# Kernel optimization log

Measured on AMD Instinct MI355X. Metric: run time of the kernel, lower is better.

The kernel has to match this reference:

```python
import math
import jax, jax.numpy as jnp
import numpy as np

NUM_HEADS = 16
NEG = -1e30  # block-causal 'invisible' value (stand-in for -inf)
SCALES = [(1, 1, 1), (1, 2, 2), (1, 4, 4), (1, 8, 8), (1, 16, 16), (1, 32, 32)]


def _block_causal_bias(L):
    blocks = np.array([t * h * w for (t, h, w) in SCALES])
    cum = np.cumsum(blocks)  # visible kv length for each scale block
    per_query_visible = np.repeat(cum, blocks)  # (L,)
    cols = np.arange(L)
    mask = np.where(cols[None, :] < per_query_visible[:, None], 0.0, NEG).astype(np.float32)
    return jnp.asarray(mask)[None, None]  # (1,1,L,L)


def _rope_tables(L, half_dim):
    # 2D-rope-style cos/sin tables; exact frequency layout is data, math is the rotation
    pos = np.arange(L, dtype=np.float32)
    inv_freq = 1.0 / (10000.0 ** (np.arange(half_dim, dtype=np.float32) / half_dim))
    ang = pos[:, None] * inv_freq[None, :]  # (L, half_dim)
    return jnp.asarray(np.cos(ang)), jnp.asarray(np.sin(ang))


def setup_inputs() -> dict:
    key = jax.random.key(0)
    ks = jax.random.split(key, 6)
    B, C, H = 4, 1024, NUM_HEADS
    hd = C // H
    L = int(sum(t * h * w for (t, h, w) in SCALES))  # 1365
    x = jax.random.normal(ks[0], (B, L, C), dtype=jnp.float32)
    attn_bias = _block_causal_bias(L)
    rope_cos, rope_sin = _rope_tables(L, hd // 2)
    W_qkv = jax.random.normal(ks[1], (3 * C, C), dtype=jnp.float32) * (C ** -0.5)
    q_bias = jnp.zeros((C,), dtype=jnp.float32)
    v_bias = jnp.zeros((C,), dtype=jnp.float32)
    scale_mul_log = jnp.full((1, H, 1, 1), math.log(4.0), dtype=jnp.float32)
    W_proj = jax.random.normal(ks[2], (C, C), dtype=jnp.float32) * (C ** -0.5)
    b_proj = jnp.zeros((C,), dtype=jnp.float32)
    return {"x": x, "attn_bias": attn_bias, "rope_cos": rope_cos, "rope_sin": rope_sin,
            "W_qkv": W_qkv, "q_bias": q_bias, "v_bias": v_bias,
            "scale_mul_log": scale_mul_log, "W_proj": W_proj, "b_proj": b_proj}


def _apply_rope(t, rope_cos, rope_sin):
    # t: (B,H,L,hd) -> rotate consecutive pairs with per-position cos/sin
    B, H, L, hd = t.shape
    t2 = t.reshape(B, H, L, hd // 2, 2)
    c = rope_cos[None, None]  # (1,1,L,hd/2)
    s = rope_sin[None, None]
    r0 = c * t2[..., 0] - s * t2[..., 1]
    r1 = s * t2[..., 0] + c * t2[..., 1]
    return jnp.stack([r0, r1], axis=-1).reshape(B, H, L, hd)


def reference(x, attn_bias, rope_cos, rope_sin, W_qkv, q_bias, v_bias,
              scale_mul_log, W_proj, b_proj):
    B, L, C = x.shape
    H = NUM_HEADS
    hd = C // H
    # QKV with custom bias construction: (q_bias, zeros, v_bias)
    bias = jnp.concatenate([q_bias, jnp.zeros_like(q_bias), v_bias])
    qkv = (x @ W_qkv.T + bias).reshape(B, L, 3, H, hd)
    qkv = jnp.transpose(qkv, (2, 0, 3, 1, 4))  # (3,B,H,L,hd)
    q, k, v = qkv[0], qkv[1], qkv[2]
    # cos-attn: L2-normalize q,k; q scaled by clamped learnable per-head temperature
    max_scale_mul = math.log(100.0)
    scale_mul = jnp.exp(jnp.minimum(scale_mul_log, max_scale_mul))  # (1,H,1,1)
    q = q / jnp.maximum(jnp.linalg.norm(q, axis=-1, keepdims=True), 1e-12) * scale_mul
    k = k / jnp.maximum(jnp.linalg.norm(k, axis=-1, keepdims=True), 1e-12)
    # inline RoPE on q and k
    q = _apply_rope(q, rope_cos, rope_sin)
    k = _apply_rope(k, rope_cos, rope_sin)
    # block-causal attention; softmax scale = 1 under cos_attn
    logits = jnp.einsum('bhqd,bhkd->bhqk', q, k) + attn_bias
    attn = jax.nn.softmax(logits, axis=-1)
    out = jnp.einsum('bhqk,bhkd->bhqd', attn, v)
    out = jnp.transpose(out, (0, 2, 1, 3)).reshape(B, L, C)
    return out @ W_proj.T + b_proj
```

## Files before the change

### kernel.cpp

```cpp
#include <hip/hip_runtime.h>

typedef __bf16 bf16_t;
typedef __bf16 bf16x8 __attribute__((ext_vector_type(8)));
typedef float f32x4 __attribute__((ext_vector_type(4)));

#define B_SZ 4
#define NHEADS 16
#define L_SEQ 1365
#define LP_V 1408
#define C_DIM 1024
#define HD 64
#define M_ROWS (B_SZ * L_SEQ)
#define K_DIM 1024
#define BHL (B_SZ * NHEADS * L_SEQ)

#define NSPLIT 33
#define NCHUNK 2
#define UPB (10 + NSPLIT * NCHUNK)
#define NBLK_ATTN (64 * UPB / 4)

__device__ __forceinline__ f32x4 zero4() {
    f32x4 z; z[0] = 0.f; z[1] = 0.f; z[2] = 0.f; z[3] = 0.f; return z;
}

__device__ __forceinline__ void gload_lds16(const void* g, void* l) {
    __builtin_amdgcn_global_load_lds(
        (const __attribute__((address_space(1))) void*)(uintptr_t)g,
        (__attribute__((address_space(3))) void*)(unsigned int)(uintptr_t)l,
        16, 0, 0);
}

__device__ __forceinline__ int vislen(int row) {
    if (row < 1) return 1;
    if (row < 5) return 5;
    if (row < 21) return 21;
    if (row < 85) return 85;
    if (row < 341) return 341;
    return 1365;
}

#define N8_X  (5591040 / 8)
#define N8_WQ (3145728 / 8)
#define N8_WP (1048576 / 8)
__global__ __launch_bounds__(256) void cvt_all(const float* __restrict__ x,
                                               const float* __restrict__ wq,
                                               const float* __restrict__ wp,
                                               bf16_t* __restrict__ xo,
                                               bf16_t* __restrict__ wqo,
                                               bf16_t* __restrict__ wpo) {
    int i = blockIdx.x * 256 + threadIdx.x;
    const float* in;
    bf16_t* out;
    if (i < N8_X) { in = x; out = xo; }
    else if (i < N8_X + N8_WQ) { i -= N8_X; in = wq; out = wqo; }
    else if (i < N8_X + N8_WQ + N8_WP) { i -= N8_X + N8_WQ; in = wp; out = wpo; }
    else return;
    const float* p = in + (size_t)i * 8;
    f32x4 a = *(const f32x4*)p;
    f32x4 b = *(const f32x4*)(p + 4);
    bf16x8 r;
    r[0] = (bf16_t)a[0]; r[1] = (bf16_t)a[1]; r[2] = (bf16_t)a[2]; r[3] = (bf16_t)a[3];
    r[4] = (bf16_t)b[0]; r[5] = (bf16_t)b[1]; r[6] = (bf16_t)b[2]; r[7] = (bf16_t)b[3];
    *(bf16x8*)(out + (size_t)i * 8) = r;
}

__global__ __launch_bounds__(256) void qkv_gemm(const bf16_t* __restrict__ A,
                                                const bf16_t* __restrict__ Bw,
                                                const float* __restrict__ qbias,
                                                const float* __restrict__ vbias,
                                                const float* __restrict__ rc,
                                                const float* __restrict__ rs,
                                                const float* __restrict__ sml,
                                                bf16_t* __restrict__ qo,
                                                bf16_t* __restrict__ ko,
                                                bf16_t* __restrict__ vt) {
    __shared__ __align__(16) bf16_t As[128 * 32];
    __shared__ __align__(16) bf16_t Bs[128 * 32];
    const int tid = threadIdx.x;
    const int w = tid >> 6, lane = tid & 63, quad = lane >> 4, l16 = lane & 15;
    const int id = blockIdx.x;
    const int xcd = id & 7, s = id >> 3;
    const int ntile = xcd * 3 + s / 43;
    const int mtile = s - (s / 43) * 43;
    const int mw = (w >> 1) * 64, nw = (w & 1) * 64;

    int ar0 = mtile * 128 + (tid >> 2); if (ar0 > M_ROWS - 1) ar0 = M_ROWS - 1;
    int ar1 = ar0 + 64;                 if (ar1 > M_ROWS - 1) ar1 = M_ROWS - 1;
    const int nr0 = ntile * 128 + (tid >> 2);
    const int cc = (tid & 3) * 8;

    f32x4 acc[4][4];
#pragma unroll
    for (int i = 0; i < 4; ++i)
#pragma unroll
        for (int j = 0; j < 4; ++j) acc[i][j] = zero4();

    for (int k0 = 0; k0 < K_DIM; k0 += 32) {
        __syncthreads();
        gload_lds16(A + (size_t)ar0 * K_DIM + k0 + cc, (char*)As + tid * 16);
        gload_lds16(A + (size_t)ar1 * K_DIM + k0 + cc, (char*)As + tid * 16 + 4096);
        gload_lds16(Bw + (size_t)nr0 * K_DIM + k0 + cc, (char*)Bs + tid * 16);
        gload_lds16(Bw + (size_t)(nr0 + 64) * K_DIM + k0 + cc, (char*)Bs + tid * 16 + 4096);
        __syncthreads();
        bf16x8 af[4], bfr[4];
#pragma unroll
        for (int mi = 0; mi < 4; ++mi)
            af[mi] = *(const bf16x8*)&As[(mw + mi * 16 + l16) * 32 + quad * 8];
#pragma unroll
        for (int ni = 0; ni < 4; ++ni)
            bfr[ni] = *(const bf16x8*)&Bs[(nw + ni * 16 + l16) * 32 + quad * 8];
#pragma unroll
        for (int mi = 0; mi < 4; ++mi)
#pragma unroll
            for (int ni = 0; ni < 4; ++ni)
                acc[mi][ni] = __builtin_amdgcn_mfma_f32_16x16x32_bf16(af[mi], bfr[ni], acc[mi][ni], 0, 0, 0);
    }

    const int three = ntile >> 3;
    const int h = (((ntile & 7) * 128 + nw) >> 6);

    if (three == 2) {
#pragma unroll
        for (int ni = 0; ni < 4; ++ni) {
            int d = ni * 16 + l16;
            float bv = vbias[h * 64 + d];
#pragma unroll
            for (int mi = 0; mi < 4; ++mi)
#pragma unroll
                for (int r = 0; r < 4; ++r) {
                    int grow = mtile * 128 + mw + mi * 16 + quad * 4 + r;
                    if (grow < M_ROWS) {
                        int b_ = grow / L_SEQ;
                        int l = grow - b_ * L_SEQ;
                        vt[(((size_t)(b_ * NHEADS + h)) * L_SEQ + l) * HD + d] =
                            (bf16_t)(acc[mi][ni][r] + bv);
                    }
                }
        }
    } else {
        float scale = 1.f;
        if (three == 0) scale = __expf(fminf(sml[h], 4.6051702f));
        float bias[4];
#pragma unroll
        for (int ni = 0; ni < 4; ++ni)
            bias[ni] = (three == 0) ? qbias[h * 64 + ni * 16 + l16] : 0.f;
        bf16_t* dst = (three == 0) ? qo : ko;
#pragma unroll
        for (int mi = 0; mi < 4; ++mi)
#pragma unroll
            for (int r = 0; r < 4; ++r) {
                int grow = mtile * 128 + mw + mi * 16 + quad * 4 + r;
                float vv[4];
                float ss = 0.f;
#pragma unroll
                for (int ni = 0; ni < 4; ++ni) {
                    vv[ni] = acc[mi][ni][r] + bias[ni];
                    ss += vv[ni] * vv[ni];
                }
                ss += __shfl_xor(ss, 1); ss += __shfl_xor(ss, 2);
                ss += __shfl_xor(ss, 4); ss += __shfl_xor(ss, 8);
                float inv = scale * rsqrtf(fmaxf(ss, 1e-24f));
                int gc = grow < M_ROWS ? grow : M_ROWS - 1;
                int b_ = gc / L_SEQ;
                int l = gc - b_ * L_SEQ;
#pragma unroll
                for (int ni = 0; ni < 4; ++ni) {
                    float vn = vv[ni] * inv;
                    float pp = __shfl_xor(vn, 1);
                    int ti = l * 32 + ni * 8 + (l16 >> 1);
                    float c = rc[ti], s2 = rs[ti];
                    float ov = (l16 & 1) ? (s2 * pp + c * vn) : (c * vn - s2 * pp);
                    if (grow < M_ROWS)
                        dst[(((size_t)(b_ * NHEADS + h)) * L_SEQ + l) * HD + ni * 16 + l16] =
                            (bf16_t)ov;
                }
            }
    }
}

__global__ __launch_bounds__(256) void vtrans(const bf16_t* __restrict__ in,
                                              bf16_t* __restrict__ out) {
    __shared__ bf16_t t[64][64];
    const int lt = blockIdx.x * 64, bh = blockIdx.y;
    const int tid = threadIdx.x;
#pragma unroll
    for (int it = 0; it < 2; ++it) {
        const int r = (tid >> 3) + it * 32, c8 = (tid & 7) * 8;
        int l = lt + r; if (l > L_SEQ - 1) l = L_SEQ - 1;
        bf16x8 v8 = *(const bf16x8*)(in + ((size_t)bh * L_SEQ + l) * HD + c8);
#pragma unroll
        for (int j = 0; j < 8; ++j) t[c8 + j][r] = v8[j];
    }
    __syncthreads();
#pragma unroll
    for (int it = 0; it < 2; ++it) {
        int c = tid + it * 256;
        int d = c >> 3, off = (c & 7) * 8;
        bf16x8 o8 = *(const bf16x8*)&t[d][off];
        *(bf16x8*)(out + ((size_t)bh * HD + d) * LP_V + lt + off) = o8;
    }
}

__global__ __launch_bounds__(256) void attn(const bf16_t* __restrict__ q,
                                            const bf16_t* __restrict__ k,
                                            const bf16_t* __restrict__ v,
                                            bf16_t* __restrict__ ao,
                                            float* __restrict__ OP,
                                            float* __restrict__ LPb) {
    __shared__ __align__(16) bf16_t plds[4][2][16][72];
    const int tid = threadIdx.x;
    const int w = tid >> 6, lane = tid & 63, quad = lane >> 4, l16 = lane & 15;
    const int bid = blockIdx.x;
    const int xcd = bid & 7, s0 = bid >> 3;
    const int bh = (xcd << 3) + s0 / 19;
    const int ublk = s0 - (s0 / 19) * 19;
    const int u = ublk * 4 + w;
    int g, t0, t1, ck = 0;
    bool direct;
    if (u < 10) { g = u; t0 = 0; t1 = (u < 2) ? 2 : 6; direct = true; }
    else {
        int t = u - 10;
        int gi = t >> 1;
        ck = t & 1;
        g = 10 + gi;
        t0 = ck * 11;
        t1 = t0 + 11;
        direct = false;
    }
    const int qbase = g * 32;

    bf16x8 aq[2][2];
#pragma unroll
    for (int h = 0; h < 2; ++h) {
        int mrow = qbase + h * 16 + l16;
        int mc = mrow < L_SEQ ? mrow : (L_SEQ - 1);
        const bf16_t* qp = q + ((size_t)bh * L_SEQ + mc) * HD + quad * 8;
        aq[h][0] = *(const bf16x8*)(qp);
        aq[h][1] = *(const bf16x8*)(qp + 32);
    }

    f32x4 o[2][4];
    float l_i[2][4];
    int visr[2][4];
#pragma unroll
    for (int h = 0; h < 2; ++h)
#pragma unroll
        for (int r = 0; r < 4; ++r) {
            o[h][r] = zero4();
            l_i[h][r] = 0.f;
            visr[h][r] = vislen(qbase + h * 16 + quad * 4 + r);
        }

    for (int kt = t0; kt < t1; ++kt) {
        const int kvb = kt * 64;
        bf16x8 kf0[4], kf1[4];
#pragma unroll
        for (int nb = 0; nb < 4; ++nb) {
            int n = kvb + nb * 16 + l16;
            int nc = n < L_SEQ ? n : (L_SEQ - 1);
            const bf16_t* kp = k + ((size_t)bh * L_SEQ + nc) * HD + quad * 8;
            kf0[nb] = *(const bf16x8*)(kp);
            kf1[nb] = *(const bf16x8*)(kp + 32);
        }
        f32x4 s[2][4];
#pragma unroll
        for (int h = 0; h < 2; ++h)
#pragma unroll
            for (int nb = 0; nb < 4; ++nb) {
                s[h][nb] = zero4();
                s[h][nb] = __builtin_amdgcn_mfma_f32_16x16x32_bf16(aq[h][0], kf0[nb], s[h][nb], 0, 0, 0);
                s[h][nb] = __builtin_amdgcn_mfma_f32_16x16x32_bf16(aq[h][1], kf1[nb], s[h][nb], 0, 0, 0);
            }

#pragma unroll
        for (int h = 0; h < 2; ++h)
#pragma unroll
            for (int nb = 0; nb < 4; ++nb) {
                int col = kvb + nb * 16 + l16;
#pragma unroll
                for (int r = 0; r < 4; ++r) {
                    float e = __expf(s[h][nb][r]);
                    float p = (col < visr[h][r]) ? e : 0.f;
                    l_i[h][r] += p;
                    plds[w][h][quad * 4 + r][nb * 16 + l16] = (bf16_t)p;
                }
            }
        bf16x8 ap[2][2];
#pragma unroll
        for (int h = 0; h < 2; ++h) {
            ap[h][0] = *(const bf16x8*)&plds[w][h][l16][quad * 8];
            ap[h][1] = *(const bf16x8*)&plds[w][h][l16][32 + quad * 8];
        }
#pragma unroll
        for (int nb = 0; nb < 4; ++nb) {
            const bf16_t* vp = v + ((size_t)bh * HD + nb * 16 + l16) * LP_V + kvb + quad * 8;
            bf16x8 v0 = *(const bf16x8*)(vp);
            bf16x8 v1 = *(const bf16x8*)(vp + 32);
#pragma unroll
            for (int h = 0; h < 2; ++h) {
                o[h][nb] = __builtin_amdgcn_mfma_f32_16x16x32_bf16(ap[h][0], v0, o[h][nb], 0, 0, 0);
                o[h][nb] = __builtin_amdgcn_mfma_f32_16x16x32_bf16(ap[h][1], v1, o[h][nb], 0, 0, 0);
            }
        }
    }

    if (direct) {
        const int b_ = bh >> 4, hh = bh & 15;
#pragma unroll
        for (int h = 0; h < 2; ++h)
#pragma unroll
            for (int r = 0; r < 4; ++r) {
                float ls = l_i[h][r];
#pragma unroll
                for (int off = 1; off < 16; off <<= 1) ls += __shfl_xor(ls, off);
                int rowq = qbase + h * 16 + quad * 4 + r;
                if (rowq < L_SEQ) {
                    float inv = 1.f / ls;
#pragma unroll
                    for (int nb = 0; nb < 4; ++nb) {
                        int d = nb * 16 + l16;
                        size_t di = ((size_t)(b_ * L_SEQ + rowq)) * C_DIM + hh * HD + d;
                        ao[di] = (bf16_t)(o[h][nb][r] * inv);
                    }
                }
            }
    } else {
        const int g9 = g - 10;
        size_t ub = (((size_t)ck * 64 + bh) * NSPLIT + g9) * 2048;
#pragma unroll
        for (int h = 0; h < 2; ++h)
#pragma unroll
            for (int nb = 0; nb < 4; ++nb)
                *(f32x4*)(OP + ub + (size_t)((h * 4 + nb) * 64 + lane) * 4) = o[h][nb];
        size_t lb = (((size_t)ck * 64 + bh) * NSPLIT + g9) * 32;
#pragma unroll
        for (int h = 0; h < 2; ++h)
#pragma unroll
            for (int r = 0; r < 4; ++r) {
                float ls = l_i[h][r];
#pragma unroll
                for (int off = 1; off < 16; off <<= 1) ls += __shfl_xor(ls, off);
                if (l16 == 0) LPb[lb + h * 16 + quad * 4 + r] = ls;
            }
    }
}

__global__ __launch_bounds__(256) void attn_reduce(const float* __restrict__ OP,
                                                   const float* __restrict__ LPb,
                                                   bf16_t* __restrict__ ao) {
    __shared__ float lsum[32];
    const int bid = blockIdx.x;
    const int xcd = bid & 7, s = bid >> 3;
    const int bh = (xcd << 3) + s / 33;
    const int g9 = s - (s / 33) * 33;
    const int tid = threadIdx.x;
    if (tid < 32) {
        float sm = 0.f;
#pragma unroll
        for (int ck = 0; ck < NCHUNK; ++ck)
            sm += LPb[(((size_t)ck * 64 + bh) * NSPLIT + g9) * 32 + tid];
        lsum[tid] = sm;
    }
    __syncthreads();
    const int lane = tid & 63, p = tid >> 6;
    const int quad = lane >> 4, l16 = lane & 15;
    const int qbase = (g9 + 10) * 32;
    const int b_ = bh >> 4, hh = bh & 15;
    size_t ub = ((size_t)bh * NSPLIT + g9) * 2048;
#pragma unroll
    for (int h = 0; h < 2; ++h) {
        f32x4 acc = zero4();
#pragma unroll
        for (int ck = 0; ck < NCHUNK; ++ck)
            acc += *(const f32x4*)(OP + (size_t)ck * 64 * NSPLIT * 2048 + ub +
                                   (size_t)((h * 4 + p) * 64 + lane) * 4);
        int col = p * 16 + l16;
#pragma unroll
        for (int r = 0; r < 4; ++r) {
            int row = h * 16 + quad * 4 + r;
            int rowq = qbase + row;
            if (rowq < L_SEQ)
                ao[((size_t)(b_ * L_SEQ + rowq)) * C_DIM + hh * HD + col] =
                    (bf16_t)(acc[r] / lsum[row]);
        }
    }
}

__global__ __launch_bounds__(256) void proj_gemm(const bf16_t* __restrict__ A,
                                                 const bf16_t* __restrict__ Bw,
                                                 const float* __restrict__ bias,
                                                 float* __restrict__ out) {
    __shared__ __align__(16) bf16_t As[128 * 32];
    __shared__ __align__(16) bf16_t Bs[128 * 32];
    const int tid = threadIdx.x;
    const int w = tid >> 6, lane = tid & 63, quad = lane >> 4, l16 = lane & 15;
    const int id = blockIdx.x;
    const int ntile = id & 7, mtile = id >> 3;
    const int mw = (w >> 1) * 64, nw = (w & 1) * 64;

    int ar0 = mtile * 128 + (tid >> 2); if (ar0 > M_ROWS - 1) ar0 = M_ROWS - 1;
    int ar1 = ar0 + 64;                 if (ar1 > M_ROWS - 1) ar1 = M_ROWS - 1;
    const int nr0 = ntile * 128 + (tid >> 2);
    const int cc = (tid & 3) * 8;

    f32x4 acc[4][4];
#pragma unroll
    for (int i = 0; i < 4; ++i)
#pragma unroll
        for (int j = 0; j < 4; ++j) acc[i][j] = zero4();

    for (int k0 = 0; k0 < K_DIM; k0 += 32) {
        __syncthreads();
        gload_lds16(A + (size_t)ar0 * K_DIM + k0 + cc, (char*)As + tid * 16);
        gload_lds16(A + (size_t)ar1 * K_DIM + k0 + cc, (char*)As + tid * 16 + 4096);
        gload_lds16(Bw + (size_t)nr0 * K_DIM + k0 + cc, (char*)Bs + tid * 16);
        gload_lds16(Bw + (size_t)(nr0 + 64) * K_DIM + k0 + cc, (char*)Bs + tid * 16 + 4096);
        __syncthreads();
        bf16x8 af[4], bfr[4];
#pragma unroll
        for (int mi = 0; mi < 4; ++mi)
            af[mi] = *(const bf16x8*)&As[(mw + mi * 16 + l16) * 32 + quad * 8];
#pragma unroll
        for (int ni = 0; ni < 4; ++ni)
            bfr[ni] = *(const bf16x8*)&Bs[(nw + ni * 16 + l16) * 32 + quad * 8];
#pragma unroll
        for (int mi = 0; mi < 4; ++mi)
#pragma unroll
            for (int ni = 0; ni < 4; ++ni)
                acc[mi][ni] = __builtin_amdgcn_mfma_f32_16x16x32_bf16(af[mi], bfr[ni], acc[mi][ni], 0, 0, 0);
    }

#pragma unroll
    for (int ni = 0; ni < 4; ++ni) {
        int ncol = ntile * 128 + nw + ni * 16 + l16;
        float bv = bias[ncol];
#pragma unroll
        for (int mi = 0; mi < 4; ++mi)
#pragma unroll
            for (int r = 0; r < 4; ++r) {
                int grow = mtile * 128 + mw + mi * 16 + quad * 4 + r;
                if (grow < M_ROWS)
                    out[(size_t)grow * C_DIM + ncol] = acc[mi][ni][r] + bv;
            }
    }
}

extern "C" void kernel_launch(void* const* d_in, const int* in_sizes, int n_in,
                              void* d_out, int out_size, void* d_ws, size_t ws_size,
                              hipStream_t stream) {
    const float* x    = (const float*)d_in[0];
    const float* rc   = (const float*)d_in[2];
    const float* rs   = (const float*)d_in[3];
    const float* Wqkv = (const float*)d_in[4];
    const float* qb   = (const float*)d_in[5];
    const float* vb   = (const float*)d_in[6];
    const float* sml  = (const float*)d_in[7];
    const float* Wp   = (const float*)d_in[8];
    const float* bp   = (const float*)d_in[9];
    float* out = (float*)d_out;

    const size_t NQ   = (size_t)B_SZ * NHEADS * L_SEQ * HD;
    const size_t NVT  = (size_t)B_SZ * NHEADS * HD * LP_V;
    const size_t NX   = (size_t)M_ROWS * C_DIM;
    const size_t NWQ  = (size_t)3 * C_DIM * C_DIM;
    const size_t NWP  = (size_t)C_DIM * C_DIM;

    bf16_t* qo   = (bf16_t*)d_ws;
    bf16_t* ko   = qo + NQ;
    bf16_t* vtmp = ko + NQ;
    bf16_t* vo   = vtmp + NQ;
    bf16_t* xb   = vo + NVT;
    bf16_t* ao   = xb;
    bf16_t* wqb  = xb + NX;
    bf16_t* wpb  = wqb + NWQ;
    float*  OPb  = (float*)(wpb + NWP);
    float*  LPb  = OPb + (size_t)NCHUNK * 64 * NSPLIT * 2048;

    dim3 blk(256);
    const int ncvt = (N8_X + N8_WQ + N8_WP + 255) / 256;
    cvt_all<<<dim3(ncvt), blk, 0, stream>>>(x, Wqkv, Wp, xb, wqb, wpb);
    qkv_gemm<<<dim3(1032), blk, 0, stream>>>(xb, wqb, qb, vb, rc, rs, sml, qo, ko, vtmp);
    vtrans<<<dim3(22, 64), blk, 0, stream>>>(vtmp, vo);
    attn<<<dim3(NBLK_ATTN), blk, 0, stream>>>(qo, ko, vo, ao, OPb, LPb);
    attn_reduce<<<dim3(2112), blk, 0, stream>>>(OPb, LPb, ao);
    proj_gemm<<<dim3(344), blk, 0, stream>>>(ao, wpb, bp, out);
}
```

Measured before the change: 346.3 us.

## Replace split-KV attention plus reduce with single-pass 16-row query tiles

Attention work units move from 32-row query tiles with a two-chunk KV split (partials written to fp32 scratch, then merged by a separate reduce kernel) to 16-row tiles that each walk their whole visible KV range in one wave. This drops the attn_reduce launch and the partial-output traffic through global memory. It also adds a fast path that skips the visibility mask on fully visible KV tiles, and computes per-tile KV extent from the block-causal structure. In exchange, every K/V fragment is loaded from global once per 16 query rows instead of once per 32. Load balance is now uneven, since late query groups run up to 22 KV tiles serially, and with 22 groups per wave index some waves exit immediately.

Result: slower. 417.6 us (+20.6%).

```diff
diff --git a/kernel.cpp b/kernel.cpp
--- a/kernel.cpp
+++ b/kernel.cpp
@@ -13,11 +13,6 @@
 #define M_ROWS (B_SZ * L_SEQ)
 #define K_DIM 1024
 #define BHL (B_SZ * NHEADS * L_SEQ)
-
-#define NSPLIT 33
-#define NCHUNK 2
-#define UPB (10 + NSPLIT * NCHUNK)
-#define NBLK_ATTN (64 * UPB / 4)
 
 __device__ __forceinline__ f32x4 zero4() {
     f32x4 z; z[0] = 0.f; z[1] = 0.f; z[2] = 0.f; z[3] = 0.f; return z;
@@ -204,184 +199,107 @@
 __global__ __launch_bounds__(256) void attn(const bf16_t* __restrict__ q,
                                             const bf16_t* __restrict__ k,
                                             const bf16_t* __restrict__ v,
-                                            bf16_t* __restrict__ ao,
-                                            float* __restrict__ OP,
-                                            float* __restrict__ LPb) {
-    __shared__ __align__(16) bf16_t plds[4][2][16][72];
+                                            bf16_t* __restrict__ ao) {
+    __shared__ __align__(16) bf16_t plds[4][16][72];
     const int tid = threadIdx.x;
     const int w = tid >> 6, lane = tid & 63, quad = lane >> 4, l16 = lane & 15;
     const int bid = blockIdx.x;
     const int xcd = bid & 7, s0 = bid >> 3;
-    const int bh = (xcd << 3) + s0 / 19;
-    const int ublk = s0 - (s0 / 19) * 19;
-    const int u = ublk * 4 + w;
-    int g, t0, t1, ck = 0;
-    bool direct;
-    if (u < 10) { g = u; t0 = 0; t1 = (u < 2) ? 2 : 6; direct = true; }
-    else {
-        int t = u - 10;
-        int gi = t >> 1;
-        ck = t & 1;
-        g = 10 + gi;
-        t0 = ck * 11;
-        t1 = t0 + 11;
-        direct = false;
-    }
-    const int qbase = g * 32;
-
-    bf16x8 aq[2][2];
-#pragma unroll
-    for (int h = 0; h < 2; ++h) {
-        int mrow = qbase + h * 16 + l16;
-        int mc = mrow < L_SEQ ? mrow : (L_SEQ - 1);
-        const bf16_t* qp = q + ((size_t)bh * L_SEQ + mc) * HD + quad * 8;
-        aq[h][0] = *(const bf16x8*)(qp);
-        aq[h][1] = *(const bf16x8*)(qp + 32);
-    }
-
-    f32x4 o[2][4];
-    float l_i[2][4];
-    int visr[2][4];
-#pragma unroll
-    for (int h = 0; h < 2; ++h)
-#pragma unroll
-        for (int r = 0; r < 4; ++r) {
-            o[h][r] = zero4();
-            l_i[h][r] = 0.f;
-            visr[h][r] = vislen(qbase + h * 16 + quad * 4 + r);
-        }
-
-    for (int kt = t0; kt < t1; ++kt) {
+    const int bh = (xcd << 3) + s0 / 22;
+    const int gblk = s0 - (s0 / 22) * 22;
+    const int g = gblk + 22 * w;
+    if (g >= 86) return;
+    const int qbase = g * 16;
+
+    int mrow = qbase + l16;
+    int mc = mrow < L_SEQ ? mrow : (L_SEQ - 1);
+    const bf16_t* qp = q + ((size_t)bh * L_SEQ + mc) * HD + quad * 8;
+    bf16x8 aq0 = *(const bf16x8*)(qp);
+    bf16x8 aq1 = *(const bf16x8*)(qp + 32);
+
+    f32x4 o[4];
+    o[0] = zero4(); o[1] = zero4(); o[2] = zero4(); o[3] = zero4();
+    float l_i[4] = {0.f, 0.f, 0.f, 0.f};
+    int visr[4];
+#pragma unroll
+    for (int r = 0; r < 4; ++r) visr[r] = vislen(qbase + quad * 4 + r);
+    const int minvis = vislen(qbase);
+
+    int rl = qbase + 15; if (rl > L_SEQ - 1) rl = L_SEQ - 1;
+    const int ntk = (vislen(rl) + 63) >> 6;
+
+    const bf16_t* kb = k + (size_t)bh * L_SEQ * HD + (size_t)l16 * HD + quad * 8;
+    const bf16_t* vb = v + ((size_t)bh * HD + l16) * LP_V + quad * 8;
+
+    for (int kt = 0; kt < ntk; ++kt) {
         const int kvb = kt * 64;
+        const bf16_t* kp = kb + (size_t)kvb * HD;
         bf16x8 kf0[4], kf1[4];
 #pragma unroll
         for (int nb = 0; nb < 4; ++nb) {
-            int n = kvb + nb * 16 + l16;
-            int nc = n < L_SEQ ? n : (L_SEQ - 1);
-            const bf16_t* kp = k + ((size_t)bh * L_SEQ + nc) * HD + quad * 8;
-            kf0[nb] = *(const bf16x8*)(kp);
-            kf1[nb] = *(const bf16x8*)(kp + 32);
-        }
-        f32x4 s[2][4];
-#pragma unroll
-        for (int h = 0; h < 2; ++h)
-#pragma unroll
-            for (int nb = 0; nb < 4; ++nb) {
-                s[h][nb] = zero4();
-                s[h][nb] = __builtin_amdgcn_mfma_f32_16x16x32_bf16(aq[h][0], kf0[nb], s[h][nb], 0, 0, 0);
-                s[h][nb] = __builtin_amdgcn_mfma_f32_16x16x32_bf16(aq[h][1], kf1[nb], s[h][nb], 0, 0, 0);
-            }
-
-#pragma unroll
-        for (int h = 0; h < 2; ++h)
+            kf0[nb] = *(const bf16x8*)(kp + nb * (16 * HD));
+            kf1[nb] = *(const bf16x8*)(kp + nb * (16 * HD) + 32);
+        }
+        f32x4 s[4];
+#pragma unroll
+        for (int nb = 0; nb < 4; ++nb) {
+            s[nb] = zero4();
+            s[nb] = __builtin_amdgcn_mfma_f32_16x16x32_bf16(aq0, kf0[nb], s[nb], 0, 0, 0);
+            s[nb] = __builtin_amdgcn_mfma_f32_16x16x32_bf16(aq1, kf1[nb], s[nb], 0, 0, 0);
+        }
+
+        if (kvb + 64 <= minvis) {
+#pragma unroll
+            for (int nb = 0; nb < 4; ++nb)
+#pragma unroll
+                for (int r = 0; r < 4; ++r) {
+                    float p = __expf(s[nb][r]);
+                    l_i[r] += p;
+                    plds[w][quad * 4 + r][nb * 16 + l16] = (bf16_t)p;
+                }
+        } else {
 #pragma unroll
             for (int nb = 0; nb < 4; ++nb) {
                 int col = kvb + nb * 16 + l16;
 #pragma unroll
                 for (int r = 0; r < 4; ++r) {
-                    float e = __expf(s[h][nb][r]);
-                    float p = (col < visr[h][r]) ? e : 0.f;
-                    l_i[h][r] += p;
-                    plds[w][h][quad * 4 + r][nb * 16 + l16] = (bf16_t)p;
+                    float e = __expf(s[nb][r]);
+                    float p = (col < visr[r]) ? e : 0.f;
+                    l_i[r] += p;
+                    plds[w][quad * 4 + r][nb * 16 + l16] = (bf16_t)p;
                 }
             }
-        bf16x8 ap[2][2];
-#pragma unroll
-        for (int h = 0; h < 2; ++h) {
-            ap[h][0] = *(const bf16x8*)&plds[w][h][l16][quad * 8];
-            ap[h][1] = *(const bf16x8*)&plds[w][h][l16][32 + quad * 8];
-        }
+        }
+
+        bf16x8 ap0 = *(const bf16x8*)&plds[w][l16][quad * 8];
+        bf16x8 ap1 = *(const bf16x8*)&plds[w][l16][32 + quad * 8];
+
+        const bf16_t* vp = v + ((size_t)bh * HD) * LP_V + kvb + quad * 8;
 #pragma unroll
         for (int nb = 0; nb < 4; ++nb) {
-            const bf16_t* vp = v + ((size_t)bh * HD + nb * 16 + l16) * LP_V + kvb + quad * 8;
-            bf16x8 v0 = *(const bf16x8*)(vp);
-            bf16x8 v1 = *(const bf16x8*)(vp + 32);
-#pragma unroll
-            for (int h = 0; h < 2; ++h) {
-                o[h][nb] = __builtin_amdgcn_mfma_f32_16x16x32_bf16(ap[h][0], v0, o[h][nb], 0, 0, 0);
-                o[h][nb] = __builtin_amdgcn_mfma_f32_16x16x32_bf16(ap[h][1], v1, o[h][nb], 0, 0, 0);
+            const bf16_t* vpn = vp + (size_t)(nb * 16 + l16) * LP_V;
+            bf16x8 v0 = *(const bf16x8*)(vpn);
+            bf16x8 v1 = *(const bf16x8*)(vpn + 32);
+            o[nb] = __builtin_amdgcn_mfma_f32_16x16x32_bf16(ap0, v0, o[nb], 0, 0, 0);
+            o[nb] = __builtin_amdgcn_mfma_f32_16x16x32_bf16(ap1, v1, o[nb], 0, 0, 0);
+        }
+    }
+
+    const int b_ = bh >> 4, hh = bh & 15;
+#pragma unroll
+    for (int r = 0; r < 4; ++r) {
+        float ls = l_i[r];
+#pragma unroll
+        for (int off = 1; off < 16; off <<= 1) ls += __shfl_xor(ls, off);
+        int rowq = qbase + quad * 4 + r;
+        if (rowq < L_SEQ) {
+            float inv = 1.f / ls;
+#pragma unroll
+            for (int nb = 0; nb < 4; ++nb) {
+                int d = nb * 16 + l16;
+                size_t di = ((size_t)(b_ * L_SEQ + rowq)) * C_DIM + hh * HD + d;
+                ao[di] = (bf16_t)(o[nb][r] * inv);
             }
-        }
-    }
-
-    if (direct) {
-        const int b_ = bh >> 4, hh = bh & 15;
-#pragma unroll
-        for (int h = 0; h < 2; ++h)
-#pragma unroll
-            for (int r = 0; r < 4; ++r) {
-                float ls = l_i[h][r];
-#pragma unroll
-                for (int off = 1; off < 16; off <<= 1) ls += __shfl_xor(ls, off);
-                int rowq = qbase + h * 16 + quad * 4 + r;
-                if (rowq < L_SEQ) {
-                    float inv = 1.f / ls;
-#pragma unroll
-                    for (int nb = 0; nb < 4; ++nb) {
-                        int d = nb * 16 + l16;
-                        size_t di = ((size_t)(b_ * L_SEQ + rowq)) * C_DIM + hh * HD + d;
-                        ao[di] = (bf16_t)(o[h][nb][r] * inv);
-                    }
-                }
-            }
-    } else {
-        const int g9 = g - 10;
-        size_t ub = (((size_t)ck * 64 + bh) * NSPLIT + g9) * 2048;
-#pragma unroll
-        for (int h = 0; h < 2; ++h)
-#pragma unroll
-            for (int nb = 0; nb < 4; ++nb)
-                *(f32x4*)(OP + ub + (size_t)((h * 4 + nb) * 64 + lane) * 4) = o[h][nb];
-        size_t lb = (((size_t)ck * 64 + bh) * NSPLIT + g9) * 32;
-#pragma unroll
-        for (int h = 0; h < 2; ++h)
-#pragma unroll
-            for (int r = 0; r < 4; ++r) {
-                float ls = l_i[h][r];
-#pragma unroll
-                for (int off = 1; off < 16; off <<= 1) ls += __shfl_xor(ls, off);
-                if (l16 == 0) LPb[lb + h * 16 + quad * 4 + r] = ls;
-            }
-    }
-}
-
-__global__ __launch_bounds__(256) void attn_reduce(const float* __restrict__ OP,
-                                                   const float* __restrict__ LPb,
-                                                   bf16_t* __restrict__ ao) {
-    __shared__ float lsum[32];
-    const int bid = blockIdx.x;
-    const int xcd = bid & 7, s = bid >> 3;
-    const int bh = (xcd << 3) + s / 33;
-    const int g9 = s - (s / 33) * 33;
-    const int tid = threadIdx.x;
-    if (tid < 32) {
-        float sm = 0.f;
-#pragma unroll
-        for (int ck = 0; ck < NCHUNK; ++ck)
-            sm += LPb[(((size_t)ck * 64 + bh) * NSPLIT + g9) * 32 + tid];
-        lsum[tid] = sm;
-    }
-    __syncthreads();
-    const int lane = tid & 63, p = tid >> 6;
-    const int quad = lane >> 4, l16 = lane & 15;
-    const int qbase = (g9 + 10) * 32;
-    const int b_ = bh >> 4, hh = bh & 15;
-    size_t ub = ((size_t)bh * NSPLIT + g9) * 2048;
-#pragma unroll
-    for (int h = 0; h < 2; ++h) {
-        f32x4 acc = zero4();
-#pragma unroll
-        for (int ck = 0; ck < NCHUNK; ++ck)
-            acc += *(const f32x4*)(OP + (size_t)ck * 64 * NSPLIT * 2048 + ub +
-                                   (size_t)((h * 4 + p) * 64 + lane) * 4);
-        int col = p * 16 + l16;
-#pragma unroll
-        for (int r = 0; r < 4; ++r) {
-            int row = h * 16 + quad * 4 + r;
-            int rowq = qbase + row;
-            if (rowq < L_SEQ)
-                ao[((size_t)(b_ * L_SEQ + rowq)) * C_DIM + hh * HD + col] =
-                    (bf16_t)(acc[r] / lsum[row]);
         }
     }
 }
@@ -473,15 +391,12 @@
     bf16_t* ao   = xb;
     bf16_t* wqb  = xb + NX;
     bf16_t* wpb  = wqb + NWQ;
-    float*  OPb  = (float*)(wpb + NWP);
-    float*  LPb  = OPb + (size_t)NCHUNK * 64 * NSPLIT * 2048;
 
     dim3 blk(256);
     const int ncvt = (N8_X + N8_WQ + N8_WP + 255) / 256;
     cvt_all<<<dim3(ncvt), blk, 0, stream>>>(x, Wqkv, Wp, xb, wqb, wpb);
     qkv_gemm<<<dim3(1032), blk, 0, stream>>>(xb, wqb, qb, vb, rc, rs, sml, qo, ko, vtmp);
     vtrans<<<dim3(22, 64), blk, 0, stream>>>(vtmp, vo);
-    attn<<<dim3(NBLK_ATTN), blk, 0, stream>>>(qo, ko, vo, ao, OPb, LPb);
-    attn_reduce<<<dim3(2112), blk, 0, stream>>>(OPb, LPb, ao);
+    attn<<<dim3(1408), blk, 0, stream>>>(qo, ko, vo, ao);
     proj_gemm<<<dim3(344), blk, 0, stream>>>(ao, wpb, bp, out);
 }
```

## Share K/V tiles in LDS across 128-row query blocks and drop split-KV reduce

Applied to the files above, without the earlier changes.

Each block now handles 128 query rows of one head, four waves of 32 rows each. The block cooperatively stages every 64-row K and V tile into shared memory instead of each wave reading K/V from global memory on its own. This removes the split-KV partitioning, the fp32 partial-output buffers and the separate attn_reduce kernel. A mask-free fast path handles tiles that lie entirely inside the visible range. The trade-off is worse load balance: blocks covering late query rows loop over up to 22 KV tiles while early blocks do very little. Barriers are also added on every tile iteration.

New measurement: 279.6 us. 1.24x faster.

```diff
diff --git a/kernel.cpp b/kernel.cpp
--- a/kernel.cpp
+++ b/kernel.cpp
@@ -13,11 +13,6 @@
 #define M_ROWS (B_SZ * L_SEQ)
 #define K_DIM 1024
 #define BHL (B_SZ * NHEADS * L_SEQ)
-
-#define NSPLIT 33
-#define NCHUNK 2
-#define UPB (10 + NSPLIT * NCHUNK)
-#define NBLK_ATTN (64 * UPB / 4)
 
 __device__ __forceinline__ f32x4 zero4() {
     f32x4 z; z[0] = 0.f; z[1] = 0.f; z[2] = 0.f; z[3] = 0.f; return z;
@@ -204,30 +199,17 @@
 __global__ __launch_bounds__(256) void attn(const bf16_t* __restrict__ q,
                                             const bf16_t* __restrict__ k,
                                             const bf16_t* __restrict__ v,
-                                            bf16_t* __restrict__ ao,
-                                            float* __restrict__ OP,
-                                            float* __restrict__ LPb) {
+                                            bf16_t* __restrict__ ao) {
+    __shared__ __align__(16) bf16_t Ks[64][72];
+    __shared__ __align__(16) bf16_t Vs[64][72];
     __shared__ __align__(16) bf16_t plds[4][2][16][72];
     const int tid = threadIdx.x;
     const int w = tid >> 6, lane = tid & 63, quad = lane >> 4, l16 = lane & 15;
     const int bid = blockIdx.x;
     const int xcd = bid & 7, s0 = bid >> 3;
-    const int bh = (xcd << 3) + s0 / 19;
-    const int ublk = s0 - (s0 / 19) * 19;
-    const int u = ublk * 4 + w;
-    int g, t0, t1, ck = 0;
-    bool direct;
-    if (u < 10) { g = u; t0 = 0; t1 = (u < 2) ? 2 : 6; direct = true; }
-    else {
-        int t = u - 10;
-        int gi = t >> 1;
-        ck = t & 1;
-        g = 10 + gi;
-        t0 = ck * 11;
-        t1 = t0 + 11;
-        direct = false;
-    }
-    const int qbase = g * 32;
+    const int bh = (xcd << 3) + s0 / 11;
+    const int qg = s0 - (s0 / 11) * 11;
+    const int qbase = qg * 128 + w * 32;
 
     bf16x8 aq[2][2];
 #pragma unroll
@@ -250,17 +232,34 @@
             l_i[h][r] = 0.f;
             visr[h][r] = vislen(qbase + h * 16 + quad * 4 + r);
         }
-
-    for (int kt = t0; kt < t1; ++kt) {
+    const int minvis = vislen(qbase);
+
+    int rl = qg * 128 + 127; if (rl > L_SEQ - 1) rl = L_SEQ - 1;
+    const int ntk = (vislen(rl) + 63) >> 6;
+
+    const int srow = tid >> 2;
+    const int scol = (tid & 3) * 16;
+
+    for (int kt = 0; kt < ntk; ++kt) {
         const int kvb = kt * 64;
+        const bf16_t* kp = k + ((size_t)bh * L_SEQ + kvb + srow) * HD + scol;
+        const bf16_t* vp = v + ((size_t)bh * HD + srow) * LP_V + kvb + scol;
+        bf16x8 k0 = *(const bf16x8*)(kp);
+        bf16x8 k1 = *(const bf16x8*)(kp + 8);
+        bf16x8 v0 = *(const bf16x8*)(vp);
+        bf16x8 v1 = *(const bf16x8*)(vp + 8);
+        __syncthreads();
+        *(bf16x8*)&Ks[srow][scol] = k0;
+        *(bf16x8*)&Ks[srow][scol + 8] = k1;
+        *(bf16x8*)&Vs[srow][scol] = v0;
+        *(bf16x8*)&Vs[srow][scol + 8] = v1;
+        __syncthreads();
+
         bf16x8 kf0[4], kf1[4];
 #pragma unroll
         for (int nb = 0; nb < 4; ++nb) {
-            int n = kvb + nb * 16 + l16;
-            int nc = n < L_SEQ ? n : (L_SEQ - 1);
-            const bf16_t* kp = k + ((size_t)bh * L_SEQ + nc) * HD + quad * 8;
-            kf0[nb] = *(const bf16x8*)(kp);
-            kf1[nb] = *(const bf16x8*)(kp + 32);
+            kf0[nb] = *(const bf16x8*)&Ks[nb * 16 + l16][quad * 8];
+            kf1[nb] = *(const bf16x8*)&Ks[nb * 16 + l16][32 + quad * 8];
         }
         f32x4 s[2][4];
 #pragma unroll
@@ -272,19 +271,33 @@
                 s[h][nb] = __builtin_amdgcn_mfma_f32_16x16x32_bf16(aq[h][1], kf1[nb], s[h][nb], 0, 0, 0);
             }
 
-#pragma unroll
-        for (int h = 0; h < 2; ++h)
-#pragma unroll
-            for (int nb = 0; nb < 4; ++nb) {
-                int col = kvb + nb * 16 + l16;
-#pragma unroll
-                for (int r = 0; r < 4; ++r) {
-                    float e = __expf(s[h][nb][r]);
-                    float p = (col < visr[h][r]) ? e : 0.f;
-                    l_i[h][r] += p;
-                    plds[w][h][quad * 4 + r][nb * 16 + l16] = (bf16_t)p;
+        if (kvb + 64 <= minvis) {
+#pragma unroll
+            for (int h = 0; h < 2; ++h)
+#pragma unroll
+                for (int nb = 0; nb < 4; ++nb)
+#pragma unroll
+                    for (int r = 0; r < 4; ++r) {
+                        float p = __expf(s[h][nb][r]);
+                        l_i[h][r] += p;
+                        plds[w][h][quad * 4 + r][nb * 16 + l16] = (bf16_t)p;
+                    }
+        } else {
+#pragma unroll
+            for (int h = 0; h < 2; ++h)
+#pragma unroll
+                for (int nb = 0; nb < 4; ++nb) {
+                    int col = kvb + nb * 16 + l16;
+#pragma unroll
+                    for (int r = 0; r < 4; ++r) {
+                        float e = __expf(s[h][nb][r]);
+                        float p = (col < visr[h][r]) ? e : 0.f;
+                        l_i[h][r] += p;
+                        plds[w][h][quad * 4 + r][nb * 16 + l16] = (bf16_t)p;
+                    }
                 }
-            }
+        }
+
         bf16x8 ap[2][2];
 #pragma unroll
         for (int h = 0; h < 2; ++h) {
@@ -293,97 +306,35 @@
         }
 #pragma unroll
         for (int nb = 0; nb < 4; ++nb) {
-            const bf16_t* vp = v + ((size_t)bh * HD + nb * 16 + l16) * LP_V + kvb + quad * 8;
-            bf16x8 v0 = *(const bf16x8*)(vp);
-            bf16x8 v1 = *(const bf16x8*)(vp + 32);
+            bf16x8 vf0 = *(const bf16x8*)&Vs[nb * 16 + l16][quad * 8];
+            bf16x8 vf1 = *(const bf16x8*)&Vs[nb * 16 + l16][32 + quad * 8];
 #pragma unroll
             for (int h = 0; h < 2; ++h) {
-                o[h][nb] = __builtin_amdgcn_mfma_f32_16x16x32_bf16(ap[h][0], v0, o[h][nb], 0, 0, 0);
-                o[h][nb] = __builtin_amdgcn_mfma_f32_16x16x32_bf16(ap[h][1], v1, o[h][nb], 0, 0, 0);
+                o[h][nb] = __builtin_amdgcn_mfma_f32_16x16x32_bf16(ap[h][0], vf0, o[h][nb], 0, 0, 0);
+                o[h][nb] = __builtin_amdgcn_mfma_f32_16x16x32_bf16(ap[h][1], vf1, o[h][nb], 0, 0, 0);
             }
         }
     }
 
-    if (direct) {
-        const int b_ = bh >> 4, hh = bh & 15;
-#pragma unroll
-        for (int h = 0; h < 2; ++h)
-#pragma unroll
-            for (int r = 0; r < 4; ++r) {
-                float ls = l_i[h][r];
-#pragma unroll
-                for (int off = 1; off < 16; off <<= 1) ls += __shfl_xor(ls, off);
-                int rowq = qbase + h * 16 + quad * 4 + r;
-                if (rowq < L_SEQ) {
-                    float inv = 1.f / ls;
-#pragma unroll
-                    for (int nb = 0; nb < 4; ++nb) {
-                        int d = nb * 16 + l16;
-                        size_t di = ((size_t)(b_ * L_SEQ + rowq)) * C_DIM + hh * HD + d;
-                        ao[di] = (bf16_t)(o[h][nb][r] * inv);
-                    }
+    const int b_ = bh >> 4, hh = bh & 15;
+#pragma unroll
+    for (int h = 0; h < 2; ++h)
+#pragma unroll
+        for (int r = 0; r < 4; ++r) {
+            float ls = l_i[h][r];
+#pragma unroll
+            for (int off = 1; off < 16; off <<= 1) ls += __shfl_xor(ls, off);
+            int rowq = qbase + h * 16 + quad * 4 + r;
+            if (rowq < L_SEQ) {
+                float inv = 1.f / ls;
+#pragma unroll
+                for (int nb = 0; nb < 4; ++nb) {
+                    int d = nb * 16 + l16;
+                    size_t di = ((size_t)(b_ * L_SEQ + rowq)) * C_DIM + hh * HD + d;
+                    ao[di] = (bf16_t)(o[h][nb][r] * inv);
                 }
             }
-    } else {
-        const int g9 = g - 10;
-        size_t ub = (((size_t)ck * 64 + bh) * NSPLIT + g9) * 2048;
-#pragma unroll
-        for (int h = 0; h < 2; ++h)
-#pragma unroll
-            for (int nb = 0; nb < 4; ++nb)
-                *(f32x4*)(OP + ub + (size_t)((h * 4 + nb) * 64 + lane) * 4) = o[h][nb];
-        size_t lb = (((size_t)ck * 64 + bh) * NSPLIT + g9) * 32;
-#pragma unroll
-        for (int h = 0; h < 2; ++h)
-#pragma unroll
-            for (int r = 0; r < 4; ++r) {
-                float ls = l_i[h][r];
-#pragma unroll
-                for (int off = 1; off < 16; off <<= 1) ls += __shfl_xor(ls, off);
-                if (l16 == 0) LPb[lb + h * 16 + quad * 4 + r] = ls;
-            }
-    }
-}
-
-__global__ __launch_bounds__(256) void attn_reduce(const float* __restrict__ OP,
-                                                   const float* __restrict__ LPb,
-                                                   bf16_t* __restrict__ ao) {
-    __shared__ float lsum[32];
-    const int bid = blockIdx.x;
-    const int xcd = bid & 7, s = bid >> 3;
-    const int bh = (xcd << 3) + s / 33;
-    const int g9 = s - (s / 33) * 33;
-    const int tid = threadIdx.x;
-    if (tid < 32) {
-        float sm = 0.f;
-#pragma unroll
-        for (int ck = 0; ck < NCHUNK; ++ck)
-            sm += LPb[(((size_t)ck * 64 + bh) * NSPLIT + g9) * 32 + tid];
-        lsum[tid] = sm;
-    }
-    __syncthreads();
-    const int lane = tid & 63, p = tid >> 6;
-    const int quad = lane >> 4, l16 = lane & 15;
-    const int qbase = (g9 + 10) * 32;
-    const int b_ = bh >> 4, hh = bh & 15;
-    size_t ub = ((size_t)bh * NSPLIT + g9) * 2048;
-#pragma unroll
-    for (int h = 0; h < 2; ++h) {
-        f32x4 acc = zero4();
-#pragma unroll
-        for (int ck = 0; ck < NCHUNK; ++ck)
-            acc += *(const f32x4*)(OP + (size_t)ck * 64 * NSPLIT * 2048 + ub +
-                                   (size_t)((h * 4 + p) * 64 + lane) * 4);
-        int col = p * 16 + l16;
-#pragma unroll
-        for (int r = 0; r < 4; ++r) {
-            int row = h * 16 + quad * 4 + r;
-            int rowq = qbase + row;
-            if (rowq < L_SEQ)
-                ao[((size_t)(b_ * L_SEQ + rowq)) * C_DIM + hh * HD + col] =
-                    (bf16_t)(acc[r] / lsum[row]);
-        }
-    }
+        }
 }
 
 __global__ __launch_bounds__(256) void proj_gemm(const bf16_t* __restrict__ A,
@@ -473,15 +424,12 @@
     bf16_t* ao   = xb;
     bf16_t* wqb  = xb + NX;
     bf16_t* wpb  = wqb + NWQ;
-    float*  OPb  = (float*)(wpb + NWP);
-    float*  LPb  = OPb + (size_t)NCHUNK * 64 * NSPLIT * 2048;
 
     dim3 blk(256);
     const int ncvt = (N8_X + N8_WQ + N8_WP + 255) / 256;
     cvt_all<<<dim3(ncvt), blk, 0, stream>>>(x, Wqkv, Wp, xb, wqb, wpb);
     qkv_gemm<<<dim3(1032), blk, 0, stream>>>(xb, wqb, qb, vb, rc, rs, sml, qo, ko, vtmp);
     vtrans<<<dim3(22, 64), blk, 0, stream>>>(vtmp, vo);
-    attn<<<dim3(NBLK_ATTN), blk, 0, stream>>>(qo, ko, vo, ao, OPb, LPb);
-    attn_reduce<<<dim3(2112), blk, 0, stream>>>(OPb, LPb, ao);
+    attn<<<dim3(704), blk, 0, stream>>>(qo, ko, vo, ao);
     proj_gemm<<<dim3(344), blk, 0, stream>>>(ao, wpb, bp, out);
 }
```
